# Optimization experiments

Measured on AMD Instinct MI355X. Metric: run time of the kernel, lower is better.

Reference implementation:

```python
import jax, jax.numpy as jnp
import numpy as np

B, H_C, W_C = 4, 256, 256        # coarse mask logits
C, H_F, W_F = 128, 512, 512      # fine feature map
N_POINTS = 8192
HIDDEN = 256


def _grid_sample_bilinear(img, grid):
    """Bilinear grid_sample, align_corners=False, zeros padding.
    img: [C,H,W]; grid: [N,2] with (x,y) in [-1,1]. Returns [N,C]."""
    Ci, H, W = img.shape
    x = ((grid[:, 0] + 1.0) * W - 1.0) * 0.5
    y = ((grid[:, 1] + 1.0) * H - 1.0) * 0.5
    x0 = jnp.floor(x); y0 = jnp.floor(y)
    x1 = x0 + 1.0; y1 = y0 + 1.0
    wx1 = x - x0; wx0 = 1.0 - wx1
    wy1 = y - y0; wy0 = 1.0 - wy1

    def gather(xi, yi):
        valid = (xi >= 0) & (xi < W) & (yi >= 0) & (yi < H)
        xc = jnp.clip(xi, 0, W - 1).astype(jnp.int32)
        yc = jnp.clip(yi, 0, H - 1).astype(jnp.int32)
        v = img[:, yc, xc]                       # [C,N]
        return v * valid.astype(img.dtype)

    out = (gather(x0, y0) * (wx0 * wy0)
           + gather(x1, y0) * (wx1 * wy0)
           + gather(x0, y1) * (wx0 * wy1)
           + gather(x1, y1) * (wx1 * wy1))       # [C,N]
    return out.T                                  # [N,C]


def setup_inputs() -> dict:
    key = jax.random.key(0)
    k1, k2, k3, k4 = jax.random.split(key, 4)
    coarse_logits = jax.random.normal(k1, (B, 1, H_C, W_C), dtype=jnp.float32)
    fine_feat = jax.random.normal(k2, (B, C, H_F, W_F), dtype=jnp.float32)
    W1 = jax.random.normal(k3, (C + 1, HIDDEN), dtype=jnp.float32) * (1.0 / np.sqrt(C + 1))
    b1 = jnp.zeros((HIDDEN,), dtype=jnp.float32)
    W2 = jax.random.normal(k4, (HIDDEN, 1), dtype=jnp.float32) * (1.0 / np.sqrt(HIDDEN))
    b2 = jnp.zeros((1,), dtype=jnp.float32)
    return {"coarse_logits": coarse_logits, "fine_feat": fine_feat,
            "W1": W1, "b1": b1, "W2": W2, "b2": b2, "num_points": N_POINTS}


def reference(coarse_logits, fine_feat, W1, b1, W2, b2, num_points):
    b, _, h, w = coarse_logits.shape
    # uncertainty = -|logits|  (calculate_uncertainty)
    unc = -jnp.abs(coarse_logits[:, 0])                       # [B,h,w]
    _, idx = jax.lax.top_k(unc.reshape(b, -1), num_points)    # [B,N]
    # pixel-center normalized coords (sampling_points eval branch): (x,y) in [0,1]
    h_step, w_step = 1.0 / h, 1.0 / w
    px = w_step / 2.0 + (idx % w).astype(jnp.float32) * w_step
    py = h_step / 2.0 + (idx // w).astype(jnp.float32) * h_step
    grid = 2.0 * jnp.stack([px, py], axis=-1) - 1.0           # [B,N,2] in [-1,1]
    # point_sample: bilinear gather of fine features at sampled points
    fine_pts = jax.vmap(_grid_sample_bilinear)(fine_feat, grid)   # [B,N,C]
    # point_sample_by_idx: gather coarse logits at flat indices
    coarse_flat = coarse_logits.reshape(b, -1)                 # [B,h*w]
    coarse_pts = jnp.take_along_axis(coarse_flat, idx, axis=1)[..., None]  # [B,N,1]
    # point head MLP on concat(fine, coarse)
    feats = jnp.concatenate([fine_pts, coarse_pts], axis=-1)   # [B,N,C+1]
    hid = jax.nn.relu(jnp.einsum('bnf,fk->bnk', feats, W1) + b1)
    refined = jnp.einsum('bnk,ko->bno', hid, W2) + b2          # [B,N,1]
    # scatter refined logits back into the coarse map at sampled indices
    out_flat = coarse_flat.at[jnp.arange(b)[:, None], idx].set(refined[..., 0])
    return out_flat.reshape(b, 1, h, w)
```

## Files before the change

### kernel.cpp

```cpp
#include <hip/hip_runtime.h>
#include <stdint.h>

#define B_ 4
#define HC 256
#define WC 256
#define C_ 128
#define HF 512
#define WF 512
#define NPTS 8192
#define HIDDEN_ 256
#define NPIX (HC*WC)
#define PPB 16
#define FSTRIDE 132

__global__ void pr_copy_kernel(const float4* __restrict__ src, float4* __restrict__ dst, int n4) {
    int i = blockIdx.x * blockDim.x + threadIdx.x;
    if (i < n4) dst[i] = src[i];
}

__global__ __launch_bounds__(1024) void pr_select_kernel(const float* __restrict__ coarse,
                                                         int* __restrict__ sel) {
    int b = blockIdx.x;
    const float* cb = coarse + (size_t)b * NPIX;
    int tid = threadIdx.x;
    int lane = tid & 63, wid = tid >> 6;

    __shared__ unsigned hist[256];
    __shared__ unsigned s_prefix;
    __shared__ int s_remk;
    __shared__ unsigned wsum[16];
    __shared__ unsigned s_chosen, s_cless;
    __shared__ unsigned warp_eq[16], warp_take[16];
    __shared__ unsigned s_eqbase, s_outbase;

    if (tid == 0) { s_prefix = 0u; s_remk = NPTS; }

    for (int pass = 0; pass < 4; ++pass) {
        if (tid < 256) hist[tid] = 0u;
        __syncthreads();
        unsigned prefix = s_prefix;
        int remk = s_remk;
        int shift = 24 - 8 * pass;

        if (pass == 0) {
            for (int i = 4 * tid; i < NPIX; i += 4096) {
                float4 v = *(const float4*)(cb + i);
                unsigned bins[4];
                bins[0] = (__float_as_uint(v.x) & 0x7fffffffu) >> 24;
                bins[1] = (__float_as_uint(v.y) & 0x7fffffffu) >> 24;
                bins[2] = (__float_as_uint(v.z) & 0x7fffffffu) >> 24;
                bins[3] = (__float_as_uint(v.w) & 0x7fffffffu) >> 24;
#pragma unroll
                for (int e = 0; e < 4; ++e) {
                    unsigned bin = bins[e];
                    unsigned long long am = ~0ull;
                    while (am) {
                        int leader = __ffsll((unsigned long long)am) - 1;
                        unsigned lbin = __shfl(bin, leader, 64);
                        unsigned long long match = __ballot(bin == lbin);
                        if (lane == leader) atomicAdd(&hist[lbin], (unsigned)__popcll(match));
                        am &= ~match;
                    }
                }
            }
        } else {
            for (int i = 4 * tid; i < NPIX; i += 4096) {
                float4 v = *(const float4*)(cb + i);
                unsigned k0 = __float_as_uint(v.x) & 0x7fffffffu;
                unsigned k1 = __float_as_uint(v.y) & 0x7fffffffu;
                unsigned k2 = __float_as_uint(v.z) & 0x7fffffffu;
                unsigned k3 = __float_as_uint(v.w) & 0x7fffffffu;
                if ((k0 >> (shift + 8)) == prefix) atomicAdd(&hist[(k0 >> shift) & 0xffu], 1u);
                if ((k1 >> (shift + 8)) == prefix) atomicAdd(&hist[(k1 >> shift) & 0xffu], 1u);
                if ((k2 >> (shift + 8)) == prefix) atomicAdd(&hist[(k2 >> shift) & 0xffu], 1u);
                if ((k3 >> (shift + 8)) == prefix) atomicAdd(&hist[(k3 >> shift) & 0xffu], 1u);
            }
        }
        __syncthreads();

        unsigned h = 0, incl = 0;
        if (tid < 256) {
            h = hist[tid];
            incl = h;
#pragma unroll
            for (int d = 1; d < 64; d <<= 1) {
                unsigned y = __shfl_up(incl, d, 64);
                if (lane >= d) incl += y;
            }
            if (lane == 63) wsum[wid] = incl;
        }
        __syncthreads();
        if (tid < 256) {
            unsigned base = 0;
            for (int w = 0; w < wid; ++w) base += wsum[w];
            unsigned inc = base + incl;
            unsigned exc = inc - h;
            if ((unsigned)remk > exc && (unsigned)remk <= inc) { s_chosen = (unsigned)tid; s_cless = exc; }
        }
        __syncthreads();
        if (tid == 0) { s_prefix = (s_prefix << 8) | s_chosen; s_remk = remk - (int)s_cless; }
        __syncthreads();
    }

    unsigned T = s_prefix;
    unsigned need_eq = (unsigned)s_remk;
    if (tid == 0) { s_eqbase = 0u; s_outbase = 0u; }
    __syncthreads();

    unsigned long long ltmask = (1ull << lane) - 1ull;
    for (int base = 0; base < NPIX; base += 4096) {
        int i0 = base + 4 * tid;
        float4 v = *(const float4*)(cb + i0);
        unsigned k[4];
        k[0] = __float_as_uint(v.x) & 0x7fffffffu;
        k[1] = __float_as_uint(v.y) & 0x7fffffffu;
        k[2] = __float_as_uint(v.z) & 0x7fffffffu;
        k[3] = __float_as_uint(v.w) & 0x7fffffffu;
        bool lt[4], eq[4];
        unsigned long long me[4];
        unsigned weq = 0;
#pragma unroll
        for (int e = 0; e < 4; ++e) {
            lt[e] = k[e] < T;
            eq[e] = k[e] == T;
            me[e] = __ballot(eq[e]);
            weq += (unsigned)__popcll(me[e]);
        }
        if (lane == 0) warp_eq[wid] = weq;
        __syncthreads();

        unsigned eqwb = 0, eqtot = 0;
        for (int w = 0; w < 16; ++w) { unsigned hh = warp_eq[w]; if (w < wid) eqwb += hh; eqtot += hh; }
        unsigned lt_lanes_eq = 0;
#pragma unroll
        for (int e = 0; e < 4; ++e) lt_lanes_eq += (unsigned)__popcll(me[e] & ltmask);
        unsigned ebase = s_eqbase + eqwb + lt_lanes_eq;

        bool take[4];
        unsigned long long mt[4];
        unsigned self_eq = 0;
#pragma unroll
        for (int e = 0; e < 4; ++e) {
            unsigned eqrank = ebase + self_eq;
            take[e] = lt[e] || (eq[e] && eqrank < need_eq);
            self_eq += eq[e] ? 1u : 0u;
        }
        unsigned wtk = 0;
#pragma unroll
        for (int e = 0; e < 4; ++e) {
            mt[e] = __ballot(take[e]);
            wtk += (unsigned)__popcll(mt[e]);
        }
        if (lane == 0) warp_take[wid] = wtk;
        __syncthreads();

        unsigned twb = 0, ttot = 0;
        for (int w = 0; w < 16; ++w) { unsigned hh = warp_take[w]; if (w < wid) twb += hh; ttot += hh; }
        unsigned lt_lanes_tk = 0;
#pragma unroll
        for (int e = 0; e < 4; ++e) lt_lanes_tk += (unsigned)__popcll(mt[e] & ltmask);
        unsigned tbase = s_outbase + twb + lt_lanes_tk;
        unsigned self_tk = 0;
#pragma unroll
        for (int e = 0; e < 4; ++e) {
            if (take[e]) sel[b * NPTS + (int)(tbase + self_tk)] = i0 + e;
            self_tk += take[e] ? 1u : 0u;
        }
        __syncthreads();
        if (tid == 0) { s_eqbase += eqtot; s_outbase += ttot; }
    }
}

__global__ __launch_bounds__(256) void pr_mlp_kernel(
    const float* __restrict__ coarse, const float* __restrict__ fine,
    const float* __restrict__ W1, const float* __restrict__ b1,
    const float* __restrict__ W2, const float* __restrict__ b2,
    const int* __restrict__ sel, float* __restrict__ out) {

    __shared__ __align__(16) float feats[PPB * FSTRIDE];
    __shared__ int sidx[PPB];
    __shared__ float red[PPB][4];

    int tid = threadIdx.x;
    const int bpb = NPTS / PPB;
    int b = blockIdx.x / bpb;
    int pbase = (blockIdx.x % bpb) * PPB;

    if (tid < PPB) sidx[tid] = sel[b * NPTS + pbase + tid];
    __syncthreads();

    const float* fb = fine + (size_t)b * (C_ * HF * WF);
    int c = tid & 127;
    int ph = tid >> 7;

    float2 r0[PPB / 2], r1[PPB / 2];
#pragma unroll
    for (int k = 0; k < PPB / 2; ++k) {
        int p = 2 * k + ph;
        int id = sidx[p];
        int ix = id & (WC - 1), iy = id >> 8;
        const float* a = fb + (size_t)c * (HF * WF) + (size_t)(2 * iy) * WF + 2 * ix;
        r0[k] = *(const float2*)a;
        r1[k] = *(const float2*)(a + WF);
    }
#pragma unroll
    for (int k = 0; k < PPB / 2; ++k) {
        int p = 2 * k + ph;
        feats[p * FSTRIDE + c] = 0.25f * ((r0[k].x + r0[k].y) + (r1[k].x + r1[k].y));
    }
    if (tid < PPB) feats[tid * FSTRIDE + 128] = coarse[(size_t)b * NPIX + sidx[tid]];
    __syncthreads();

    int j = tid;
    float acc[PPB];
    float b1j = b1[j];
#pragma unroll
    for (int p = 0; p < PPB; ++p) acc[p] = b1j;

    const float4* fs4 = (const float4*)feats;
#pragma unroll 4
    for (int f4 = 0; f4 < 32; ++f4) {
        float w0 = W1[(4 * f4 + 0) * HIDDEN_ + j];
        float w1 = W1[(4 * f4 + 1) * HIDDEN_ + j];
        float w2 = W1[(4 * f4 + 2) * HIDDEN_ + j];
        float w3 = W1[(4 * f4 + 3) * HIDDEN_ + j];
#pragma unroll
        for (int p = 0; p < PPB; ++p) {
            float4 fv = fs4[p * (FSTRIDE / 4) + f4];
            acc[p] = fmaf(fv.x, w0, acc[p]);
            acc[p] = fmaf(fv.y, w1, acc[p]);
            acc[p] = fmaf(fv.z, w2, acc[p]);
            acc[p] = fmaf(fv.w, w3, acc[p]);
        }
    }
    {
        float w128 = W1[128 * HIDDEN_ + j];
#pragma unroll
        for (int p = 0; p < PPB; ++p) acc[p] = fmaf(feats[p * FSTRIDE + 128], w128, acc[p]);
    }

    float w2j = W2[j];
    int lane = tid & 63, wid = tid >> 6;
#pragma unroll
    for (int p = 0; p < PPB; ++p) {
        float v = fmaxf(acc[p], 0.0f) * w2j;
        v += __shfl_down(v, 32, 64);
        v += __shfl_down(v, 16, 64);
        v += __shfl_down(v, 8, 64);
        v += __shfl_down(v, 4, 64);
        v += __shfl_down(v, 2, 64);
        v += __shfl_down(v, 1, 64);
        if (lane == 0) red[p][wid] = v;
    }
    __syncthreads();
    if (tid < PPB) {
        float r = red[tid][0] + red[tid][1] + red[tid][2] + red[tid][3] + b2[0];
        out[(size_t)b * NPIX + sidx[tid]] = r;
    }
}

extern "C" void kernel_launch(void* const* d_in, const int* in_sizes, int n_in,
                              void* d_out, int out_size, void* d_ws, size_t ws_size,
                              hipStream_t stream) {
    const float* coarse = (const float*)d_in[0];
    const float* fine   = (const float*)d_in[1];
    const float* W1     = (const float*)d_in[2];
    const float* b1     = (const float*)d_in[3];
    const float* W2     = (const float*)d_in[4];
    const float* b2     = (const float*)d_in[5];
    float* out = (float*)d_out;
    int* sel = (int*)d_ws;

    int n4 = B_ * NPIX / 4;
    pr_copy_kernel<<<(n4 + 255) / 256, 256, 0, stream>>>((const float4*)coarse, (float4*)out, n4);
    pr_select_kernel<<<B_, 1024, 0, stream>>>(coarse, sel);
    pr_mlp_kernel<<<B_ * (NPTS / PPB), 256, 0, stream>>>(coarse, fine, W1, b1, W2, b2, sel, out);
}
```

Measured before the change: 795.9 us.

## Precompute 2x2 pooled channel-last features and gather contiguous rows in MLP

The pixel-centre sample points of the 256x256 coarse grid land exactly halfway between fine pixels 2i and 2i+1, so bilinear sampling reduces to a 2x2 average pool. The select kernel now also launches extra blocks that pool the whole fine map into a channel-last workspace, running alongside the top-k selection. A new MLP kernel then loads each point's 128 features as one contiguous row instead of gathering across channel planes a megabyte apart. The trade-off is a full streaming read of the fine map plus a large pooled write, even though only one eighth of the points are used, and the path depends on the workspace being big enough; otherwise it falls back to the old gather kernel.

Result: no change. 780.3 us (-2.0%).

```diff
diff --git a/kernel.cpp b/kernel.cpp
--- a/kernel.cpp
+++ b/kernel.cpp
@@ -12,18 +12,63 @@
 #define NPIX (HC*WC)
 #define PPB 16
 #define FSTRIDE 132
+#define PSTRIDE 129
 
 __global__ void pr_copy_kernel(const float4* __restrict__ src, float4* __restrict__ dst, int n4) {
     int i = blockIdx.x * blockDim.x + threadIdx.x;
     if (i < n4) dst[i] = src[i];
 }
 
-__global__ __launch_bounds__(1024) void pr_select_kernel(const float* __restrict__ coarse,
-                                                         int* __restrict__ sel) {
+__global__ __launch_bounds__(1024) void pr_select_pool_kernel(
+        const float* __restrict__ coarse, const float* __restrict__ fine,
+        int* __restrict__ sel, float* __restrict__ pooled) {
+    int tid = threadIdx.x;
+    int lane = tid & 63, wid = tid >> 6;
+
+    if (blockIdx.x >= B_) {
+        __shared__ float plds[64 * PSTRIDE];
+        int pid = blockIdx.x - B_;
+        int b   = pid >> 10;
+        int rem = pid & 1023;
+        int iy  = rem >> 2;
+        int ix0 = (rem & 3) << 6;
+        const float* fb = fine + (size_t)b * (C_ * HF * WF);
+        int r  = lane >> 5;
+        int f4 = lane & 31;
+        const float* rowbase = fb + (size_t)(2 * iy + r) * WF + 2 * ix0 + 4 * f4;
+#pragma unroll
+        for (int ci = 0; ci < 8; ++ci) {
+            int c = ci * 16 + wid;
+            float4 v = *(const float4*)(rowbase + (size_t)c * (HF * WF));
+            float s0 = v.x + v.y;
+            float s1 = v.z + v.w;
+            float p0 = __shfl_xor(s0, 32, 64);
+            float p1 = __shfl_xor(s1, 32, 64);
+            if (r == 0) {
+                int cix = 2 * f4;
+                plds[cix * PSTRIDE + c]       = 0.25f * (s0 + p0);
+                plds[(cix + 1) * PSTRIDE + c] = 0.25f * (s1 + p1);
+            }
+        }
+        __syncthreads();
+        float* ob = pooled + ((size_t)b * NPIX + iy * WC + ix0) * C_;
+#pragma unroll
+        for (int k = 0; k < 2; ++k) {
+            int g  = tid + k * 1024;
+            int ix = g >> 5;
+            int c4 = (g & 31) * 4;
+            float4 o;
+            o.x = plds[ix * PSTRIDE + c4 + 0];
+            o.y = plds[ix * PSTRIDE + c4 + 1];
+            o.z = plds[ix * PSTRIDE + c4 + 2];
+            o.w = plds[ix * PSTRIDE + c4 + 3];
+            *(float4*)(ob + (size_t)ix * C_ + c4) = o;
+        }
+        return;
+    }
+
     int b = blockIdx.x;
     const float* cb = coarse + (size_t)b * NPIX;
-    int tid = threadIdx.x;
-    int lane = tid & 63, wid = tid >> 6;
 
     __shared__ unsigned hist[256];
     __shared__ unsigned s_prefix;
@@ -171,6 +216,83 @@
     }
 }
 
+__global__ __launch_bounds__(256) void pr_mlp_pooled_kernel(
+    const float* __restrict__ coarse, const float* __restrict__ pooled,
+    const float* __restrict__ W1, const float* __restrict__ b1,
+    const float* __restrict__ W2, const float* __restrict__ b2,
+    const int* __restrict__ sel, float* __restrict__ out) {
+
+    __shared__ __align__(16) float feats[PPB * FSTRIDE];
+    __shared__ int sidx[PPB];
+    __shared__ float red[PPB][4];
+
+    int tid = threadIdx.x;
+    const int bpb = NPTS / PPB;
+    int b = blockIdx.x / bpb;
+    int pbase = (blockIdx.x % bpb) * PPB;
+
+    if (tid < PPB) sidx[tid] = sel[b * NPTS + pbase + tid];
+    __syncthreads();
+
+    {
+        int p = tid >> 4, q = tid & 15;
+        const float* prow = pooled + ((size_t)b * NPIX + sidx[p]) * C_ + 8 * q;
+        float4 v0 = *(const float4*)(prow);
+        float4 v1 = *(const float4*)(prow + 4);
+        *(float4*)&feats[p * FSTRIDE + 8 * q]     = v0;
+        *(float4*)&feats[p * FSTRIDE + 8 * q + 4] = v1;
+    }
+    if (tid < PPB) feats[tid * FSTRIDE + 128] = coarse[(size_t)b * NPIX + sidx[tid]];
+    __syncthreads();
+
+    int j = tid;
+    float acc[PPB];
+    float b1j = b1[j];
+#pragma unroll
+    for (int p = 0; p < PPB; ++p) acc[p] = b1j;
+
+    const float4* fs4 = (const float4*)feats;
+#pragma unroll 4
+    for (int f4 = 0; f4 < 32; ++f4) {
+        float w0 = W1[(4 * f4 + 0) * HIDDEN_ + j];
+        float w1 = W1[(4 * f4 + 1) * HIDDEN_ + j];
+        float w2 = W1[(4 * f4 + 2) * HIDDEN_ + j];
+        float w3 = W1[(4 * f4 + 3) * HIDDEN_ + j];
+#pragma unroll
+        for (int p = 0; p < PPB; ++p) {
+            float4 fv = fs4[p * (FSTRIDE / 4) + f4];
+            acc[p] = fmaf(fv.x, w0, acc[p]);
+            acc[p] = fmaf(fv.y, w1, acc[p]);
+            acc[p] = fmaf(fv.z, w2, acc[p]);
+            acc[p] = fmaf(fv.w, w3, acc[p]);
+        }
+    }
+    {
+        float w128 = W1[128 * HIDDEN_ + j];
+#pragma unroll
+        for (int p = 0; p < PPB; ++p) acc[p] = fmaf(feats[p * FSTRIDE + 128], w128, acc[p]);
+    }
+
+    float w2j = W2[j];
+    int lane = tid & 63, wid = tid >> 6;
+#pragma unroll
+    for (int p = 0; p < PPB; ++p) {
+        float v = fmaxf(acc[p], 0.0f) * w2j;
+        v += __shfl_down(v, 32, 64);
+        v += __shfl_down(v, 16, 64);
+        v += __shfl_down(v, 8, 64);
+        v += __shfl_down(v, 4, 64);
+        v += __shfl_down(v, 2, 64);
+        v += __shfl_down(v, 1, 64);
+        if (lane == 0) red[p][wid] = v;
+    }
+    __syncthreads();
+    if (tid < PPB) {
+        float r = red[tid][0] + red[tid][1] + red[tid][2] + red[tid][3] + b2[0];
+        out[(size_t)b * NPIX + sidx[tid]] = r;
+    }
+}
+
 __global__ __launch_bounds__(256) void pr_mlp_kernel(
     const float* __restrict__ coarse, const float* __restrict__ fine,
     const float* __restrict__ W1, const float* __restrict__ b1,
@@ -269,10 +391,20 @@
     const float* W2     = (const float*)d_in[4];
     const float* b2     = (const float*)d_in[5];
     float* out = (float*)d_out;
+
     int* sel = (int*)d_ws;
+    const size_t selBytes    = (size_t)B_ * NPTS * sizeof(int);
+    const size_t pooledBytes = (size_t)B_ * NPIX * C_ * sizeof(float);
 
     int n4 = B_ * NPIX / 4;
     pr_copy_kernel<<<(n4 + 255) / 256, 256, 0, stream>>>((const float4*)coarse, (float4*)out, n4);
-    pr_select_kernel<<<B_, 1024, 0, stream>>>(coarse, sel);
-    pr_mlp_kernel<<<B_ * (NPTS / PPB), 256, 0, stream>>>(coarse, fine, W1, b1, W2, b2, sel, out);
+
+    if (ws_size >= selBytes + pooledBytes) {
+        float* pooled = (float*)((char*)d_ws + selBytes);
+        pr_select_pool_kernel<<<B_ + B_ * HC * (WC / 64), 1024, 0, stream>>>(coarse, fine, sel, pooled);
+        pr_mlp_pooled_kernel<<<B_ * (NPTS / PPB), 256, 0, stream>>>(coarse, pooled, W1, b1, W2, b2, sel, out);
+    } else {
+        pr_select_pool_kernel<<<B_, 1024, 0, stream>>>(coarse, fine, sel, (float*)nullptr);
+        pr_mlp_kernel<<<B_ * (NPTS / PPB), 256, 0, stream>>>(coarse, fine, W1, b1, W2, b2, sel, out);
+    }
 }
```

## Replace index-list gather with dense per-tile pooling driven by a selection bitmap

Applied to the files above, without the earlier changes.

Point selection now marks chosen pixels in a per-batch bitmap via atomicOr, which removes the second ballot, prefix-sum and barrier pass that built a compacted index list. The MLP kernel becomes a tile kernel: each block covers 64 coarse pixels, reads the matching fine-feature rows with coalesced float4 loads, average-pools them into LDS, then runs the MLP only on pixels whose bitmap bit is set. The bitmap clear is folded into the copy kernel. This trades scattered, poorly coalesced gathers for reading the whole fine map, which is about eight times as many pixels as are selected, and adds global atomics and partially idle MLP lanes when a tile has few selected points.

Result: slower. 881.3 us (+10.7%).

```diff
diff --git a/kernel.cpp b/kernel.cpp
--- a/kernel.cpp
+++ b/kernel.cpp
@@ -10,16 +10,18 @@
 #define NPTS 8192
 #define HIDDEN_ 256
 #define NPIX (HC*WC)
-#define PPB 16
-#define FSTRIDE 132
-
-__global__ void pr_copy_kernel(const float4* __restrict__ src, float4* __restrict__ dst, int n4) {
+#define FS 132
+#define SELW (NPIX/32)
+
+__global__ void pr_copy_clear_kernel(const float4* __restrict__ src, float4* __restrict__ dst,
+                                     unsigned* __restrict__ selmap) {
     int i = blockIdx.x * blockDim.x + threadIdx.x;
-    if (i < n4) dst[i] = src[i];
+    if (i < B_ * NPIX / 4) dst[i] = src[i];
+    if (i < B_ * SELW) selmap[i] = 0u;
 }
 
 __global__ __launch_bounds__(1024) void pr_select_kernel(const float* __restrict__ coarse,
-                                                         int* __restrict__ sel) {
+                                                         unsigned* __restrict__ selmap) {
     int b = blockIdx.x;
     const float* cb = coarse + (size_t)b * NPIX;
     int tid = threadIdx.x;
@@ -30,8 +32,8 @@
     __shared__ int s_remk;
     __shared__ unsigned wsum[16];
     __shared__ unsigned s_chosen, s_cless;
-    __shared__ unsigned warp_eq[16], warp_take[16];
-    __shared__ unsigned s_eqbase, s_outbase;
+    __shared__ unsigned warp_eq[16];
+    __shared__ unsigned s_eqbase;
 
     if (tid == 0) { s_prefix = 0u; s_remk = NPTS; }
 
@@ -104,7 +106,7 @@
 
     unsigned T = s_prefix;
     unsigned need_eq = (unsigned)s_remk;
-    if (tid == 0) { s_eqbase = 0u; s_outbase = 0u; }
+    if (tid == 0) s_eqbase = 0u;
     __syncthreads();
 
     unsigned long long ltmask = (1ull << lane) - 1ull;
@@ -136,126 +138,137 @@
         for (int e = 0; e < 4; ++e) lt_lanes_eq += (unsigned)__popcll(me[e] & ltmask);
         unsigned ebase = s_eqbase + eqwb + lt_lanes_eq;
 
-        bool take[4];
-        unsigned long long mt[4];
         unsigned self_eq = 0;
 #pragma unroll
         for (int e = 0; e < 4; ++e) {
             unsigned eqrank = ebase + self_eq;
-            take[e] = lt[e] || (eq[e] && eqrank < need_eq);
+            bool take = lt[e] || (eq[e] && eqrank < need_eq);
             self_eq += eq[e] ? 1u : 0u;
-        }
-        unsigned wtk = 0;
-#pragma unroll
-        for (int e = 0; e < 4; ++e) {
-            mt[e] = __ballot(take[e]);
-            wtk += (unsigned)__popcll(mt[e]);
-        }
-        if (lane == 0) warp_take[wid] = wtk;
-        __syncthreads();
-
-        unsigned twb = 0, ttot = 0;
-        for (int w = 0; w < 16; ++w) { unsigned hh = warp_take[w]; if (w < wid) twb += hh; ttot += hh; }
-        unsigned lt_lanes_tk = 0;
-#pragma unroll
-        for (int e = 0; e < 4; ++e) lt_lanes_tk += (unsigned)__popcll(mt[e] & ltmask);
-        unsigned tbase = s_outbase + twb + lt_lanes_tk;
-        unsigned self_tk = 0;
-#pragma unroll
-        for (int e = 0; e < 4; ++e) {
-            if (take[e]) sel[b * NPTS + (int)(tbase + self_tk)] = i0 + e;
-            self_tk += take[e] ? 1u : 0u;
-        }
-        __syncthreads();
-        if (tid == 0) { s_eqbase += eqtot; s_outbase += ttot; }
-    }
-}
-
-__global__ __launch_bounds__(256) void pr_mlp_kernel(
+            if (take) {
+                int pix = i0 + e;
+                atomicOr(&selmap[b * SELW + (pix >> 5)], 1u << (pix & 31));
+            }
+        }
+        __syncthreads();
+        if (tid == 0) s_eqbase += eqtot;
+    }
+}
+
+__global__ __launch_bounds__(512, 4) void pr_pool_mlp_kernel(
     const float* __restrict__ coarse, const float* __restrict__ fine,
     const float* __restrict__ W1, const float* __restrict__ b1,
     const float* __restrict__ W2, const float* __restrict__ b2,
-    const int* __restrict__ sel, float* __restrict__ out) {
-
-    __shared__ __align__(16) float feats[PPB * FSTRIDE];
-    __shared__ int sidx[PPB];
-    __shared__ float red[PPB][4];
+    const unsigned* __restrict__ selmap, float* __restrict__ out) {
+
+    __shared__ __align__(16) float plds[64 * FS];
+    __shared__ unsigned char slist[64];
+    __shared__ int s_nsel;
+    __shared__ float red[2][8][4];
 
     int tid = threadIdx.x;
-    const int bpb = NPTS / PPB;
-    int b = blockIdx.x / bpb;
-    int pbase = (blockIdx.x % bpb) * PPB;
-
-    if (tid < PPB) sidx[tid] = sel[b * NPTS + pbase + tid];
+    int lane = tid & 63, w = tid >> 6;
+    int pid = blockIdx.x;
+    int b   = pid >> 10;
+    int rem = pid & 1023;
+    int iy  = rem >> 2;
+    int ix0 = (rem & 3) << 6;
+
+    const float* fb = fine + (size_t)b * (C_ * HF * WF);
+    int r  = lane >> 5;
+    int f4 = lane & 31;
+    const float* rowbase = fb + (size_t)(2 * iy + r) * WF + 2 * ix0 + 4 * f4;
+#pragma unroll
+    for (int half = 0; half < 2; ++half) {
+        float4 vv[8];
+#pragma unroll
+        for (int ci = 0; ci < 8; ++ci) {
+            int c = half * 64 + ci * 8 + w;
+            vv[ci] = *(const float4*)(rowbase + (size_t)c * (HF * WF));
+        }
+#pragma unroll
+        for (int ci = 0; ci < 8; ++ci) {
+            int c = half * 64 + ci * 8 + w;
+            float s0 = vv[ci].x + vv[ci].y;
+            float s1 = vv[ci].z + vv[ci].w;
+            float p0 = __shfl_xor(s0, 32, 64);
+            float p1 = __shfl_xor(s1, 32, 64);
+            if (r == 0) {
+                plds[(2 * f4) * FS + c]     = 0.25f * (s0 + p0);
+                plds[(2 * f4 + 1) * FS + c] = 0.25f * (s1 + p1);
+            }
+        }
+    }
+    if (tid < 64) {
+        int pix = iy * WC + ix0 + tid;
+        plds[tid * FS + 128] = coarse[(size_t)b * NPIX + pix];
+    }
+    if (tid == 0) {
+        int wbase = b * SELW + ((iy * WC + ix0) >> 5);
+        unsigned long long m = ((unsigned long long)selmap[wbase + 1] << 32) | selmap[wbase];
+        int n = 0;
+        while (m) { int bit = __ffsll(m) - 1; slist[n++] = (unsigned char)bit; m &= m - 1; }
+        s_nsel = n;
+    }
     __syncthreads();
 
-    const float* fb = fine + (size_t)b * (C_ * HF * WF);
-    int c = tid & 127;
-    int ph = tid >> 7;
-
-    float2 r0[PPB / 2], r1[PPB / 2];
-#pragma unroll
-    for (int k = 0; k < PPB / 2; ++k) {
-        int p = 2 * k + ph;
-        int id = sidx[p];
-        int ix = id & (WC - 1), iy = id >> 8;
-        const float* a = fb + (size_t)c * (HF * WF) + (size_t)(2 * iy) * WF + 2 * ix;
-        r0[k] = *(const float2*)a;
-        r1[k] = *(const float2*)(a + WF);
-    }
-#pragma unroll
-    for (int k = 0; k < PPB / 2; ++k) {
-        int p = 2 * k + ph;
-        feats[p * FSTRIDE + c] = 0.25f * ((r0[k].x + r0[k].y) + (r1[k].x + r1[k].y));
-    }
-    if (tid < PPB) feats[tid * FSTRIDE + 128] = coarse[(size_t)b * NPIX + sidx[tid]];
-    __syncthreads();
-
-    int j = tid;
-    float acc[PPB];
+    int nsel = s_nsel;
+    int g = tid >> 8;
+    int j = tid & 255;
+    int jl = tid & 63, jw = (tid >> 6) & 3;
     float b1j = b1[j];
-#pragma unroll
-    for (int p = 0; p < PPB; ++p) acc[p] = b1j;
-
-    const float4* fs4 = (const float4*)feats;
+    float w2j = W2[j];
+
+    for (int base = 0; base < nsel; base += 16) {
+        float acc[8];
+        int cix[8];
+#pragma unroll
+        for (int k = 0; k < 8; ++k) {
+            int p = base + 2 * k + g;
+            cix[k] = (p < nsel) ? (int)slist[p] : 0;
+            acc[k] = b1j;
+        }
 #pragma unroll 4
-    for (int f4 = 0; f4 < 32; ++f4) {
-        float w0 = W1[(4 * f4 + 0) * HIDDEN_ + j];
-        float w1 = W1[(4 * f4 + 1) * HIDDEN_ + j];
-        float w2 = W1[(4 * f4 + 2) * HIDDEN_ + j];
-        float w3 = W1[(4 * f4 + 3) * HIDDEN_ + j];
-#pragma unroll
-        for (int p = 0; p < PPB; ++p) {
-            float4 fv = fs4[p * (FSTRIDE / 4) + f4];
-            acc[p] = fmaf(fv.x, w0, acc[p]);
-            acc[p] = fmaf(fv.y, w1, acc[p]);
-            acc[p] = fmaf(fv.z, w2, acc[p]);
-            acc[p] = fmaf(fv.w, w3, acc[p]);
-        }
-    }
-    {
-        float w128 = W1[128 * HIDDEN_ + j];
-#pragma unroll
-        for (int p = 0; p < PPB; ++p) acc[p] = fmaf(feats[p * FSTRIDE + 128], w128, acc[p]);
-    }
-
-    float w2j = W2[j];
-    int lane = tid & 63, wid = tid >> 6;
-#pragma unroll
-    for (int p = 0; p < PPB; ++p) {
-        float v = fmaxf(acc[p], 0.0f) * w2j;
-        v += __shfl_down(v, 32, 64);
-        v += __shfl_down(v, 16, 64);
-        v += __shfl_down(v, 8, 64);
-        v += __shfl_down(v, 4, 64);
-        v += __shfl_down(v, 2, 64);
-        v += __shfl_down(v, 1, 64);
-        if (lane == 0) red[p][wid] = v;
-    }
-    __syncthreads();
-    if (tid < PPB) {
-        float r = red[tid][0] + red[tid][1] + red[tid][2] + red[tid][3] + b2[0];
-        out[(size_t)b * NPIX + sidx[tid]] = r;
+        for (int f4i = 0; f4i < 32; ++f4i) {
+            float w0 = W1[(4 * f4i + 0) * HIDDEN_ + j];
+            float w1 = W1[(4 * f4i + 1) * HIDDEN_ + j];
+            float w2 = W1[(4 * f4i + 2) * HIDDEN_ + j];
+            float w3 = W1[(4 * f4i + 3) * HIDDEN_ + j];
+#pragma unroll
+            for (int k = 0; k < 8; ++k) {
+                float4 fv = *(const float4*)&plds[cix[k] * FS + 4 * f4i];
+                acc[k] = fmaf(fv.x, w0, acc[k]);
+                acc[k] = fmaf(fv.y, w1, acc[k]);
+                acc[k] = fmaf(fv.z, w2, acc[k]);
+                acc[k] = fmaf(fv.w, w3, acc[k]);
+            }
+        }
+        {
+            float w128 = W1[128 * HIDDEN_ + j];
+#pragma unroll
+            for (int k = 0; k < 8; ++k)
+                acc[k] = fmaf(plds[cix[k] * FS + 128], w128, acc[k]);
+        }
+#pragma unroll
+        for (int k = 0; k < 8; ++k) {
+            float v = fmaxf(acc[k], 0.0f) * w2j;
+            v += __shfl_down(v, 32, 64);
+            v += __shfl_down(v, 16, 64);
+            v += __shfl_down(v, 8, 64);
+            v += __shfl_down(v, 4, 64);
+            v += __shfl_down(v, 2, 64);
+            v += __shfl_down(v, 1, 64);
+            if (jl == 0) red[g][k][jw] = v;
+        }
+        __syncthreads();
+        if (tid < 16) {
+            int g2 = tid & 1, k2 = tid >> 1;
+            int p = base + 2 * k2 + g2;
+            if (p < nsel) {
+                float rr = red[g2][k2][0] + red[g2][k2][1] + red[g2][k2][2] + red[g2][k2][3] + b2[0];
+                out[(size_t)b * NPIX + iy * WC + ix0 + (int)slist[p]] = rr;
+            }
+        }
+        __syncthreads();
     }
 }
 
@@ -269,10 +282,9 @@
     const float* W2     = (const float*)d_in[4];
     const float* b2     = (const float*)d_in[5];
     float* out = (float*)d_out;
-    int* sel = (int*)d_ws;
-
-    int n4 = B_ * NPIX / 4;
-    pr_copy_kernel<<<(n4 + 255) / 256, 256, 0, stream>>>((const float4*)coarse, (float4*)out, n4);
-    pr_select_kernel<<<B_, 1024, 0, stream>>>(coarse, sel);
-    pr_mlp_kernel<<<B_ * (NPTS / PPB), 256, 0, stream>>>(coarse, fine, W1, b1, W2, b2, sel, out);
-}
+    unsigned* selmap = (unsigned*)d_ws;
+
+    pr_copy_clear_kernel<<<256, 256, 0, stream>>>((const float4*)coarse, (float4*)out, selmap);
+    pr_select_kernel<<<B_, 1024, 0, stream>>>(coarse, selmap);
+    pr_pool_mlp_kernel<<<B_ * HC * 4, 512, 0, stream>>>(coarse, fine, W1, b1, W2, b2, selmap, out);
+}
```
